# Kernel optimization log

Hardware: AMD Instinct MI355X
Metric: run time of the kernel (lower is better)

Reference implementation:

```python
import jax, jax.numpy as jnp
import numpy as np

B, A, C, M = 8, 32768, 80, 32
VAR0, VAR1 = 0.1, 0.2          # cfg['variance']
TOPK = 50                      # pre_anchor_topk
T1 = 0.5                       # bbox_threshold
SL1_W, SL1_B = 0.75, 0.11      # smooth_l1_loss_param
ALPHA, GAMMA = 0.5, 2.0
EPS = 1e-12


def point_form(b):
    # center form (cx,cy,w,h) -> corner form (x0,y0,x1,y1)
    return jnp.concatenate([b[..., :2] - b[..., 2:] / 2,
                            b[..., :2] + b[..., 2:] / 2], axis=-1)


def decode(loc, priors):
    xy = priors[..., :2] + loc[..., :2] * VAR0 * priors[..., 2:]
    wh = priors[..., 2:] * jnp.exp(loc[..., 2:] * VAR1)
    return jnp.concatenate([xy, wh], axis=-1)  # center form


def encode(matched, priors):
    # matched: corner form, priors: center form
    g_xy = ((matched[..., :2] + matched[..., 2:]) / 2 - priors[..., :2]) / (VAR0 * priors[..., 2:])
    g_wh = jnp.log((matched[..., 2:] - matched[..., :2]) / priors[..., 2:]) / VAR1
    return jnp.concatenate([g_xy, g_wh], axis=-1)


def jaccard(a, b):
    # a: [M,4] corner, b: [A,4] corner -> IoU [M,A]
    lt = jnp.maximum(a[:, None, :2], b[None, :, :2])
    rb = jnp.minimum(a[:, None, 2:], b[None, :, 2:])
    wh = jnp.clip(rb - lt, 0.0, None)
    inter = wh[..., 0] * wh[..., 1]
    area_a = (a[:, 2] - a[:, 0]) * (a[:, 3] - a[:, 1])
    area_b = (b[:, 2] - b[:, 0]) * (b[:, 3] - b[:, 1])
    return inter / (area_a[:, None] + area_b[None, :] - inter)


def clip_st(x, lo):
    # Clip custom Function: straight-through gradient
    return x + jax.lax.stop_gradient(jnp.maximum(x, lo) - x)


def bce_log(x):
    # torch BCE clamps log at -100
    return jnp.maximum(jnp.log(jnp.clip(x, 1e-38, None)), -100.0)


def _per_image(box_reg, cls_p, tgt, lab, anchors, num_classes):
    # ---- image_box_prob (no-grad branch in original) ----
    decoded = point_form(decode(box_reg, anchors))          # [A,4]
    obi = jaccard(tgt, decoded)                             # [M,A]
    t2 = jnp.maximum(obi.max(axis=1, keepdims=True), T1 + EPS)
    obp = jnp.clip((obi - T1) / (t2 - T1), 0.0, 1.0)        # [M,A]
    # sparse per-class max over objects == segment_max on labels
    seg = jax.ops.segment_max(obp, lab, num_segments=num_classes)  # [C,A]
    image_box_prob = jax.lax.stop_gradient(jnp.maximum(seg, 0.0).T)  # [A,C]

    # ---- positive bag loss ----
    mq = jaccard(tgt, point_form(anchors))                  # [M,A]
    _, matched = jax.lax.top_k(mq, TOPK)                    # [M,K]
    cls_sel = cls_p[:, lab].T                               # [M,A] prob of own class
    matched_cls = jnp.take_along_axis(cls_sel, matched, axis=1)  # [M,K]
    pri = anchors[matched]                                  # [M,K,4]
    tgt_enc = encode(tgt[:, None, :], pri)                  # [M,K,4]
    val = tgt_enc - box_reg[matched]
    av = jnp.abs(val)
    reg_loss = SL1_W * jnp.where(av < SL1_B, 0.5 / SL1_B * val * val, av - 0.5 * SL1_B).sum(-1)
    logits = matched_cls * jnp.exp(-reg_loss)               # [M,K]
    w = 1.0 / clip_st(1.0 - logits, EPS)
    w = w / w.sum(axis=1, keepdims=True)
    bag = (w * logits).sum(axis=1)                          # [M]
    pos = -bce_log(bag)                                     # BCE(bag, 1)
    return image_box_prob, pos


def setup_inputs() -> dict:
    key = jax.random.key(0)
    k1, k2, k3, k4, k5, k6, k7 = jax.random.split(key, 7)
    box_regression = jax.random.normal(k1, (B, A, 4), jnp.float32) * 0.5
    cls_logits = jax.random.normal(k2, (B, A, C), jnp.float32) - 2.0
    a_xy = jax.random.uniform(k3, (A, 2))
    a_wh = 0.02 + 0.2 * jax.random.uniform(k4, (A, 2))
    anchors = jnp.concatenate([a_xy, a_wh], axis=-1).astype(jnp.float32)
    t_min = 0.5 * jax.random.uniform(k5, (B, M, 2))
    t_wh = 0.05 + 0.4 * jax.random.uniform(k6, (B, M, 2))
    target_boxes = jnp.concatenate([t_min, t_min + t_wh], axis=-1).astype(jnp.float32)
    labels = jax.random.randint(k7, (B, M), 0, C, dtype=jnp.int32)
    return {"box_regression": box_regression, "cls_logits": cls_logits,
            "anchors": anchors, "target_boxes": target_boxes, "labels": labels}


def reference(box_regression, cls_logits, anchors, target_boxes, labels):
    num_classes = cls_logits.shape[-1]
    cls_prob = jax.nn.sigmoid(cls_logits)                   # [B,A,C]
    box_prob, pos = jax.vmap(
        lambda br, cp, tb, lb: _per_image(br, cp, tb, lb, anchors, num_classes)
    )(box_regression, cls_prob, target_boxes, labels)       # [B,A,C], [B,M]
    positive_numels = target_boxes.shape[0] * target_boxes.shape[1]
    positive_loss = pos.sum() / max(1, positive_numels)
    p = cls_prob * (1.0 - box_prob)
    # focal_loss(p, gamma) = sum(p**gamma * BCE(p, 0)) = sum(p**gamma * -log(1-p))
    negative_loss = jnp.sum(p ** GAMMA * (-bce_log(1.0 - p))) / max(1, positive_numels * TOPK)
    return (positive_loss * ALPHA, negative_loss * (1.0 - ALPHA))
```

## Files before the change

kernel.cpp:

```cpp
#include <hip/hip_runtime.h>

#define NB 8
#define NA 32768
#define NC 80
#define NM 32
#define NK 50
#define CAP 4096
#define TB 32
#define T2_BLOCKS (TB * NB)
#define POS_BLOCKS (NB * NM)
#define F0BLKS 512
#define CORRB (NA / 256)
constexpr float VAR0 = 0.1f, VAR1 = 0.2f;
constexpr float T1f  = 0.5f;
constexpr float SL1B = 0.11f;
constexpr float SL1W = 0.75f;
constexpr float FEPS = 1e-12f;

__device__ __forceinline__ float iou_corner(float tx0, float ty0, float tx1, float ty1, float ta,
                                            float bx0, float by0, float bx1, float by1, float ba) {
  float lx = fmaxf(tx0, bx0), ly = fmaxf(ty0, by0);
  float rx = fminf(tx1, bx1), ry = fminf(ty1, by1);
  float wx = fmaxf(rx - lx, 0.f), wy = fmaxf(ry - ly, 0.f);
  float inter = wx * wy;
  return inter / (ta + ba - inter);
}

__device__ __noinline__ float anchor_iou(float4 p, float tx0, float ty0, float tx1, float ty1, float ta) {
  float hx = 0.5f * p.z, hy = 0.5f * p.w;
  float x0 = p.x - hx, y0 = p.y - hy, x1 = p.x + hx, y1 = p.y + hy;
  float ba = (x1 - x0) * (y1 - y0);
  return iou_corner(tx0, ty0, tx1, ty1, ta, x0, y0, x1, y1, ba);
}

__device__ __forceinline__ float focal_term(float s, float bp) {
  float pr = s * (1.f - bp);
  float om = fmaxf(1.f - pr, 1e-38f);
  return pr * pr * fminf(-__logf(om), 100.f);
}

__global__ void __launch_bounds__(1024) mega_kernel(const float4* __restrict__ br,
                                                    const float* __restrict__ cls,
                                                    const float4* __restrict__ anc,
                                                    const float4* __restrict__ tgt,
                                                    const int* __restrict__ labels,
                                                    unsigned* __restrict__ partmax,
                                                    unsigned* __restrict__ pairmask,
                                                    float* __restrict__ posp,
                                                    float* __restrict__ f0part) {
  __shared__ int hist[512];
  __shared__ unsigned long long cand[CAP];
  __shared__ int sel[NK];
  __shared__ int s_cnt, s_B1, s_filled;
  __shared__ unsigned char s_flag[1024];
  __shared__ unsigned s_max[NM];
  __shared__ float4 s_t[NM];
  __shared__ float s_ta[NM];
  __shared__ float swave[16];

  int bx = blockIdx.x;
  int tid = threadIdx.x;

  if (bx < T2_BLOCKS) {
    int b = bx >> 5;
    int chunk = bx & 31;
    if (tid < NM) {
      float4 t = tgt[b * NM + tid];
      s_t[tid] = t;
      s_ta[tid] = (t.z - t.x) * (t.w - t.y);
      s_max[tid] = 0u;
    }
    __syncthreads();

    int a = chunk * 1024 + tid;
    float4 p = anc[a];
    float4 l = br[(size_t)b * NA + a];
    float cx = p.x + l.x * VAR0 * p.z;
    float cy = p.y + l.y * VAR0 * p.w;
    float w = p.z * __expf(l.z * VAR1);
    float h = p.w * __expf(l.w * VAR1);
    float dx0 = cx - 0.5f * w, dy0 = cy - 0.5f * h;
    float dx1 = cx + 0.5f * w, dy1 = cy + 0.5f * h;
    float da = (dx1 - dx0) * (dy1 - dy0);

    unsigned mymask = 0u;
#pragma unroll
    for (int mm = 0; mm < NM; ++mm) {
      int m = (tid + mm) & (NM - 1);
      float4 t = s_t[m];
      float iou = iou_corner(t.x, t.y, t.z, t.w, s_ta[m], dx0, dy0, dx1, dy1, da);
      if (iou > T1f) mymask |= 1u << m;
      atomicMax(&s_max[m], __float_as_uint(iou));
    }
    pairmask[(size_t)b * NA + a] = mymask;
    __syncthreads();
    if (tid < NM)
      partmax[((size_t)b * NM + tid) * TB + chunk] = s_max[tid];

  } else if (bx < T2_BLOCKS + POS_BLOCKS) {
    int bm = bx - T2_BLOCKS;
    int b = bm >> 5;
    float4 t = tgt[bm];
    float ta = (t.z - t.x) * (t.w - t.y);

    if (tid < 512) hist[tid] = 0;
    if (tid == 0) s_cnt = 0;
    __syncthreads();

    for (int a = tid; a < NA; a += 1024) {
      float iou = anchor_iou(anc[a], t.x, t.y, t.z, t.w, ta);
      if (iou > 0.f) {
        int bin = (int)(__float_as_uint(iou) >> 21);
        atomicAdd(&hist[bin], 1);
      }
    }
    __syncthreads();

    if (tid == 0) {
      int cum = 0, b1 = 0;
      for (int bin = 511; bin >= 0; --bin) {
        cum += hist[bin];
        if (cum >= NK) { b1 = bin; break; }
      }
      s_B1 = b1;
      s_filled = cum;
    }
    __syncthreads();
    int B1 = s_B1;
    bool zero_path = (s_filled < NK);

    for (int a = tid; a < NA; a += 1024) {
      float iou = anchor_iou(anc[a], t.x, t.y, t.z, t.w, ta);
      if (iou > 0.f) {
        unsigned vb = __float_as_uint(iou);
        if ((int)(vb >> 21) >= B1) {
          int slot = atomicAdd(&s_cnt, 1);
          if (slot < CAP)
            cand[slot] = ((unsigned long long)vb << 32) | (unsigned)(~a);
        }
      }
    }
    __syncthreads();
    int n = min(s_cnt, CAP);

    for (int c = tid; c < n; c += 1024) {
      unsigned long long key = cand[c];
      int rank = 0;
      for (int j = 0; j < n; ++j) rank += (cand[j] > key);
      if (rank < NK) sel[rank] = (int)(~(unsigned)(key & 0xFFFFFFFFull));
    }
    __syncthreads();

    if (zero_path) {
      if (tid == 0) s_filled = n;
      __syncthreads();
      for (int base = 0; base < NA; base += 1024) {
        int a = base + tid;
        float iou = anchor_iou(anc[a], t.x, t.y, t.z, t.w, ta);
        s_flag[tid] = (iou == 0.f);
        __syncthreads();
        if (tid == 0) {
          for (int i = 0; i < 1024 && s_filled < NK; ++i)
            if (s_flag[i]) { sel[s_filled++] = base + i; }
        }
        __syncthreads();
        if (s_filled >= NK) break;
      }
    }

    if (tid < 64) {
      int lane = tid;
      float lg = 0.f, wr = 0.f;
      if (lane < NK) {
        int a = sel[lane];
        int lb = labels[bm];
        float4 p = anc[a];
        float4 l = br[(size_t)b * NA + a];
        float logit = cls[((size_t)b * NA + a) * NC + lb];
        float mc = 1.f / (1.f + __expf(-logit));
        float gx = ((t.x + t.z) * 0.5f - p.x) / (VAR0 * p.z);
        float gy = ((t.y + t.w) * 0.5f - p.y) / (VAR0 * p.w);
        float gw = __logf((t.z - t.x) / p.z) / VAR1;
        float gh = __logf((t.w - t.y) / p.w) / VAR1;
        float v0 = gx - l.x, v1 = gy - l.y, v2 = gw - l.z, v3 = gh - l.w;
        float rl = 0.f;
        {
          float av;
          av = fabsf(v0); rl += (av < SL1B) ? (0.5f / SL1B) * v0 * v0 : (av - 0.5f * SL1B);
          av = fabsf(v1); rl += (av < SL1B) ? (0.5f / SL1B) * v1 * v1 : (av - 0.5f * SL1B);
          av = fabsf(v2); rl += (av < SL1B) ? (0.5f / SL1B) * v2 * v2 : (av - 0.5f * SL1B);
          av = fabsf(v3); rl += (av < SL1B) ? (0.5f / SL1B) * v3 * v3 : (av - 0.5f * SL1B);
        }
        rl *= SL1W;
        lg = mc * __expf(-rl);
        wr = 1.f / fmaxf(1.f - lg, FEPS);
      }
      float swl = wr * lg, swr = wr;
      for (int off = 32; off; off >>= 1) { swl += __shfl_down(swl, off); swr += __shfl_down(swr, off); }
      if (lane == 0) {
        float bag = swl / swr;
        posp[bm] = -fmaxf(logf(fmaxf(bag, 1e-38f)), -100.f);
      }
    }

  } else {
    int fb = bx - T2_BLOCKS - POS_BLOCKS;
    constexpr int NTOT4 = NB * NA * NC / 4;
    const float4* cls4 = (const float4*)cls;
    int stride = F0BLKS * 1024;
    float accum = 0.f;
    for (int i = fb * 1024 + tid; i < NTOT4; i += stride) {
      float4 v = cls4[i];
      float s0 = 1.f / (1.f + __expf(-v.x));
      float s1 = 1.f / (1.f + __expf(-v.y));
      float s2 = 1.f / (1.f + __expf(-v.z));
      float s3 = 1.f / (1.f + __expf(-v.w));
      accum += focal_term(s0, 0.f) + focal_term(s1, 0.f) +
               focal_term(s2, 0.f) + focal_term(s3, 0.f);
    }
    for (int off = 32; off; off >>= 1) accum += __shfl_down(accum, off);
    if ((tid & 63) == 0) swave[tid >> 6] = accum;
    __syncthreads();
    if (tid == 0) {
      float s = 0.f;
#pragma unroll
      for (int i = 0; i < 16; ++i) s += swave[i];
      f0part[fb] = s;
    }
  }
}

__global__ void __launch_bounds__(256) corr_kernel(const float4* __restrict__ br,
                                                   const float* __restrict__ cls,
                                                   const float4* __restrict__ anc,
                                                   const float4* __restrict__ tgt,
                                                   const int* __restrict__ labels,
                                                   const unsigned* __restrict__ partmax,
                                                   const unsigned* __restrict__ pairmask,
                                                   float* __restrict__ corrp) {
  __shared__ float4 s_t[NM];
  __shared__ float s_ta[NM], s_inv[NM];
  __shared__ unsigned s_cmask[NC];
  __shared__ unsigned s_maxm[NM];
  __shared__ unsigned s_slotmask[NM];
  __shared__ int s_slotclass[NM];
  __shared__ int s_nslots;
  int b = blockIdx.y;
  int tid = threadIdx.x;
  if (tid < NC) s_cmask[tid] = 0u;
  if (tid < NM) s_maxm[tid] = 0u;
  if (tid == 0) s_nslots = 0;
  __syncthreads();
  if (tid < NM) {
    float4 t = tgt[b * NM + tid];
    s_t[tid] = t;
    s_ta[tid] = (t.z - t.x) * (t.w - t.y);
    atomicOr(&s_cmask[labels[b * NM + tid]], 1u << tid);
  }
  {
    int m = tid >> 3, j = tid & 7;
    const unsigned* pm = &partmax[((size_t)b * NM + m) * TB];
    unsigned mx = 0u;
    for (int k = j; k < TB; k += 8) mx = max(mx, pm[k]);
    atomicMax(&s_maxm[m], mx);
  }
  __syncthreads();
  if (tid < NM) {
    float mxf = __uint_as_float(s_maxm[tid]);
    s_inv[tid] = 1.0f / (fmaxf(mxf, T1f) - T1f);
  }
  __syncthreads();
  if (tid < NC && s_cmask[tid] != 0u) {
    int slot = atomicAdd(&s_nslots, 1);
    s_slotmask[slot] = s_cmask[tid];
    s_slotclass[slot] = tid;
  }
  __syncthreads();
  int nslots = s_nslots;

  int a = blockIdx.x * 256 + tid;
  unsigned mk32 = pairmask[(size_t)b * NA + a];
  float accum = 0.f;
  if (mk32) {
    float4 p = anc[a];
    float4 l = br[(size_t)b * NA + a];
    float cx = p.x + l.x * VAR0 * p.z;
    float cy = p.y + l.y * VAR0 * p.w;
    float w = p.z * __expf(l.z * VAR1);
    float h = p.w * __expf(l.w * VAR1);
    float dx0 = cx - 0.5f * w, dy0 = cy - 0.5f * h;
    float dx1 = cx + 0.5f * w, dy1 = cy + 0.5f * h;
    float da = (dx1 - dx0) * (dy1 - dy0);
    for (int j = 0; j < nslots; ++j) {
      unsigned sm = mk32 & s_slotmask[j];
      if (!sm) continue;
      float bp = 0.f;
      while (sm) {
        int m = __ffs(sm) - 1;
        sm &= sm - 1;
        float4 t = s_t[m];
        float iou = iou_corner(t.x, t.y, t.z, t.w, s_ta[m], dx0, dy0, dx1, dy1, da);
        float o = (iou - T1f) * s_inv[m];
        bp = fmaxf(bp, fminf(fmaxf(o, 0.f), 1.f));
      }
      if (bp > 0.f) {
        float logit = cls[((size_t)b * NA + a) * NC + s_slotclass[j]];
        float s = 1.f / (1.f + __expf(-logit));
        accum += focal_term(s, bp) - focal_term(s, 0.f);
      }
    }
  }
  for (int off = 32; off; off >>= 1) accum += __shfl_down(accum, off);
  __shared__ float swv[4];
  if ((tid & 63) == 0) swv[tid >> 6] = accum;
  __syncthreads();
  if (tid == 0)
    corrp[(size_t)b * CORRB + blockIdx.x] = swv[0] + swv[1] + swv[2] + swv[3];
}

__global__ void __launch_bounds__(256) fin_kernel(const float* __restrict__ posp,
                                                  const float* __restrict__ f0part,
                                                  const float* __restrict__ corrp,
                                                  float* __restrict__ out) {
  int tid = threadIdx.x;
  double sp = 0.0, sn = 0.0;
  for (int i = tid; i < POS_BLOCKS; i += 256) sp += (double)posp[i];
  for (int i = tid; i < F0BLKS; i += 256) sn += (double)f0part[i];
  for (int i = tid; i < NB * CORRB; i += 256) sn += (double)corrp[i];
  for (int off = 32; off; off >>= 1) { sp += __shfl_down(sp, off); sn += __shfl_down(sn, off); }
  __shared__ double swp[4], swn[4];
  if ((tid & 63) == 0) { swp[tid >> 6] = sp; swn[tid >> 6] = sn; }
  __syncthreads();
  if (tid == 0) {
    double pos = swp[0] + swp[1] + swp[2] + swp[3];
    double neg = swn[0] + swn[1] + swn[2] + swn[3];
    out[0] = (float)(pos / 256.0 * 0.5);
    out[1] = (float)(neg / 12800.0 * 0.5);
  }
}

extern "C" void kernel_launch(void* const* d_in, const int* in_sizes, int n_in,
                              void* d_out, int out_size, void* d_ws, size_t ws_size,
                              hipStream_t stream) {
  const float4* br  = (const float4*)d_in[0];
  const float*  cls = (const float*)d_in[1];
  const float4* anc = (const float4*)d_in[2];
  const float4* tgt = (const float4*)d_in[3];
  const int*    lab = (const int*)d_in[4];
  float* out = (float*)d_out;
  float*    posp     = (float*)d_ws;
  float*    f0part   = (float*)((char*)d_ws + 4096);
  float*    corrp    = (float*)((char*)d_ws + 8192);
  unsigned* partmax  = (unsigned*)((char*)d_ws + 16384);
  unsigned* pairmask = (unsigned*)((char*)d_ws + 65536);

  mega_kernel<<<dim3(T2_BLOCKS + POS_BLOCKS + F0BLKS), 1024, 0, stream>>>(
      br, cls, anc, tgt, lab, partmax, pairmask, posp, f0part);
  corr_kernel<<<dim3(CORRB, NB), 256, 0, stream>>>(br, cls, anc, tgt, lab, partmax, pairmask, corrp);
  fin_kernel<<<1, 256, 0, stream>>>(posp, f0part, corrp, out);
}
```

Baseline: 60.13 us.

## Cache per-anchor IoUs in registers and schedule long positive blocks first

The positive-bag blocks now compute each anchor IoU once into a 32-entry register array and reuse it for the histogram, candidate collection and zero-fill passes, where before they recomputed it through a noinline call in each pass. The positive blocks are also moved to the front of the grid so these long-running blocks start first and overlap with the short IoU-max and focal blocks. A min-blocks hint is added to launch_bounds. The register array raises register pressure in a 1024-thread kernel that every branch shares, which may lower occupancy or cause spills.

```diff
diff --git a/kernel.cpp b/kernel.cpp
--- a/kernel.cpp
+++ b/kernel.cpp
@@ -7,8 +7,8 @@
 #define NK 50
 #define CAP 4096
 #define TB 32
+#define POS_BLOCKS (NB * NM)
 #define T2_BLOCKS (TB * NB)
-#define POS_BLOCKS (NB * NM)
 #define F0BLKS 512
 #define CORRB (NA / 256)
 constexpr float VAR0 = 0.1f, VAR1 = 0.2f;
@@ -26,28 +26,21 @@
   return inter / (ta + ba - inter);
 }
 
-__device__ __noinline__ float anchor_iou(float4 p, float tx0, float ty0, float tx1, float ty1, float ta) {
-  float hx = 0.5f * p.z, hy = 0.5f * p.w;
-  float x0 = p.x - hx, y0 = p.y - hy, x1 = p.x + hx, y1 = p.y + hy;
-  float ba = (x1 - x0) * (y1 - y0);
-  return iou_corner(tx0, ty0, tx1, ty1, ta, x0, y0, x1, y1, ba);
-}
-
 __device__ __forceinline__ float focal_term(float s, float bp) {
   float pr = s * (1.f - bp);
   float om = fmaxf(1.f - pr, 1e-38f);
   return pr * pr * fminf(-__logf(om), 100.f);
 }
 
-__global__ void __launch_bounds__(1024) mega_kernel(const float4* __restrict__ br,
-                                                    const float* __restrict__ cls,
-                                                    const float4* __restrict__ anc,
-                                                    const float4* __restrict__ tgt,
-                                                    const int* __restrict__ labels,
-                                                    unsigned* __restrict__ partmax,
-                                                    unsigned* __restrict__ pairmask,
-                                                    float* __restrict__ posp,
-                                                    float* __restrict__ f0part) {
+__global__ void __launch_bounds__(1024, 8) mega_kernel(const float4* __restrict__ br,
+                                                       const float* __restrict__ cls,
+                                                       const float4* __restrict__ anc,
+                                                       const float4* __restrict__ tgt,
+                                                       const int* __restrict__ labels,
+                                                       unsigned* __restrict__ partmax,
+                                                       unsigned* __restrict__ pairmask,
+                                                       float* __restrict__ posp,
+                                                       float* __restrict__ f0part) {
   __shared__ int hist[512];
   __shared__ unsigned long long cand[CAP];
   __shared__ int sel[NK];
@@ -61,44 +54,8 @@
   int bx = blockIdx.x;
   int tid = threadIdx.x;
 
-  if (bx < T2_BLOCKS) {
-    int b = bx >> 5;
-    int chunk = bx & 31;
-    if (tid < NM) {
-      float4 t = tgt[b * NM + tid];
-      s_t[tid] = t;
-      s_ta[tid] = (t.z - t.x) * (t.w - t.y);
-      s_max[tid] = 0u;
-    }
-    __syncthreads();
-
-    int a = chunk * 1024 + tid;
-    float4 p = anc[a];
-    float4 l = br[(size_t)b * NA + a];
-    float cx = p.x + l.x * VAR0 * p.z;
-    float cy = p.y + l.y * VAR0 * p.w;
-    float w = p.z * __expf(l.z * VAR1);
-    float h = p.w * __expf(l.w * VAR1);
-    float dx0 = cx - 0.5f * w, dy0 = cy - 0.5f * h;
-    float dx1 = cx + 0.5f * w, dy1 = cy + 0.5f * h;
-    float da = (dx1 - dx0) * (dy1 - dy0);
-
-    unsigned mymask = 0u;
-#pragma unroll
-    for (int mm = 0; mm < NM; ++mm) {
-      int m = (tid + mm) & (NM - 1);
-      float4 t = s_t[m];
-      float iou = iou_corner(t.x, t.y, t.z, t.w, s_ta[m], dx0, dy0, dx1, dy1, da);
-      if (iou > T1f) mymask |= 1u << m;
-      atomicMax(&s_max[m], __float_as_uint(iou));
-    }
-    pairmask[(size_t)b * NA + a] = mymask;
-    __syncthreads();
-    if (tid < NM)
-      partmax[((size_t)b * NM + tid) * TB + chunk] = s_max[tid];
-
-  } else if (bx < T2_BLOCKS + POS_BLOCKS) {
-    int bm = bx - T2_BLOCKS;
+  if (bx < POS_BLOCKS) {
+    int bm = bx;
     int b = bm >> 5;
     float4 t = tgt[bm];
     float ta = (t.z - t.x) * (t.w - t.y);
@@ -107,12 +64,16 @@
     if (tid == 0) s_cnt = 0;
     __syncthreads();
 
-    for (int a = tid; a < NA; a += 1024) {
-      float iou = anchor_iou(anc[a], t.x, t.y, t.z, t.w, ta);
-      if (iou > 0.f) {
-        int bin = (int)(__float_as_uint(iou) >> 21);
-        atomicAdd(&hist[bin], 1);
-      }
+    float riou[32];
+#pragma unroll
+    for (int k = 0; k < 32; ++k) {
+      float4 p = anc[tid + k * 1024];
+      float hx = 0.5f * p.z, hy = 0.5f * p.w;
+      float x0 = p.x - hx, y0 = p.y - hy, x1 = p.x + hx, y1 = p.y + hy;
+      float ba = (x1 - x0) * (y1 - y0);
+      float v = iou_corner(t.x, t.y, t.z, t.w, ta, x0, y0, x1, y1, ba);
+      riou[k] = v;
+      if (v > 0.f) atomicAdd(&hist[(int)(__float_as_uint(v) >> 21)], 1);
     }
     __syncthreads();
 
@@ -129,14 +90,15 @@
     int B1 = s_B1;
     bool zero_path = (s_filled < NK);
 
-    for (int a = tid; a < NA; a += 1024) {
-      float iou = anchor_iou(anc[a], t.x, t.y, t.z, t.w, ta);
-      if (iou > 0.f) {
-        unsigned vb = __float_as_uint(iou);
+#pragma unroll
+    for (int k = 0; k < 32; ++k) {
+      float v = riou[k];
+      if (v > 0.f) {
+        unsigned vb = __float_as_uint(v);
         if ((int)(vb >> 21) >= B1) {
           int slot = atomicAdd(&s_cnt, 1);
           if (slot < CAP)
-            cand[slot] = ((unsigned long long)vb << 32) | (unsigned)(~a);
+            cand[slot] = ((unsigned long long)vb << 32) | (unsigned)(~(tid + k * 1024));
         }
       }
     }
@@ -154,17 +116,18 @@
     if (zero_path) {
       if (tid == 0) s_filled = n;
       __syncthreads();
-      for (int base = 0; base < NA; base += 1024) {
-        int a = base + tid;
-        float iou = anchor_iou(anc[a], t.x, t.y, t.z, t.w, ta);
-        s_flag[tid] = (iou == 0.f);
-        __syncthreads();
-        if (tid == 0) {
-          for (int i = 0; i < 1024 && s_filled < NK; ++i)
-            if (s_flag[i]) { sel[s_filled++] = base + i; }
+#pragma unroll
+      for (int k = 0; k < 32; ++k) {
+        if (s_filled < NK) {
+          s_flag[tid] = (riou[k] == 0.f);
+          __syncthreads();
+          if (tid == 0) {
+            int base = k * 1024;
+            for (int i = 0; i < 1024 && s_filled < NK; ++i)
+              if (s_flag[i]) sel[s_filled++] = base + i;
+          }
+          __syncthreads();
         }
-        __syncthreads();
-        if (s_filled >= NK) break;
       }
     }
 
@@ -203,8 +166,45 @@
       }
     }
 
+  } else if (bx < POS_BLOCKS + T2_BLOCKS) {
+    int t2i = bx - POS_BLOCKS;
+    int b = t2i >> 5;
+    int chunk = t2i & 31;
+    if (tid < NM) {
+      float4 t = tgt[b * NM + tid];
+      s_t[tid] = t;
+      s_ta[tid] = (t.z - t.x) * (t.w - t.y);
+      s_max[tid] = 0u;
+    }
+    __syncthreads();
+
+    int a = chunk * 1024 + tid;
+    float4 p = anc[a];
+    float4 l = br[(size_t)b * NA + a];
+    float cx = p.x + l.x * VAR0 * p.z;
+    float cy = p.y + l.y * VAR0 * p.w;
+    float w = p.z * __expf(l.z * VAR1);
+    float h = p.w * __expf(l.w * VAR1);
+    float dx0 = cx - 0.5f * w, dy0 = cy - 0.5f * h;
+    float dx1 = cx + 0.5f * w, dy1 = cy + 0.5f * h;
+    float da = (dx1 - dx0) * (dy1 - dy0);
+
+    unsigned mymask = 0u;
+#pragma unroll
+    for (int mm = 0; mm < NM; ++mm) {
+      int m = (tid + mm) & (NM - 1);
+      float4 t = s_t[m];
+      float iou = iou_corner(t.x, t.y, t.z, t.w, s_ta[m], dx0, dy0, dx1, dy1, da);
+      if (iou > T1f) mymask |= 1u << m;
+      atomicMax(&s_max[m], __float_as_uint(iou));
+    }
+    pairmask[(size_t)b * NA + a] = mymask;
+    __syncthreads();
+    if (tid < NM)
+      partmax[((size_t)b * NM + tid) * TB + chunk] = s_max[tid];
+
   } else {
-    int fb = bx - T2_BLOCKS - POS_BLOCKS;
+    int fb = bx - POS_BLOCKS - T2_BLOCKS;
     constexpr int NTOT4 = NB * NA * NC / 4;
     const float4* cls4 = (const float4*)cls;
     int stride = F0BLKS * 1024;
@@ -354,7 +354,7 @@
   unsigned* partmax  = (unsigned*)((char*)d_ws + 16384);
   unsigned* pairmask = (unsigned*)((char*)d_ws + 65536);
 
-  mega_kernel<<<dim3(T2_BLOCKS + POS_BLOCKS + F0BLKS), 1024, 0, stream>>>(
+  mega_kernel<<<dim3(POS_BLOCKS + T2_BLOCKS + F0BLKS), 1024, 0, stream>>>(
       br, cls, anc, tgt, lab, partmax, pairmask, posp, f0part);
   corr_kernel<<<dim3(CORRB, NB), 256, 0, stream>>>(br, cls, anc, tgt, lab, partmax, pairmask, corrp);
   fin_kernel<<<1, 256, 0, stream>>>(posp, f0part, corrp, out);
```

Result: slower. 62.39 us (+3.8%).

## Distribute focal-sum streaming across all blocks before role-specific work

Applied to the files above, without the earlier changes.

The kernel no longer dedicates separate blocks to the dense focal sum. Every one of the 512 blocks now first streams a fixed slice of the class logits, with ten independent vector loads per thread, and reduces it. Each block then runs either the positive-bag or the IoU/mask work. This balances the heavy memory-bound sweep with the lighter per-anchor tasks and increases memory-level parallelism, at the cost of more registers and longer critical paths per block.

```diff
diff --git a/kernel.cpp b/kernel.cpp
--- a/kernel.cpp
+++ b/kernel.cpp
@@ -7,9 +7,7 @@
 #define NK 50
 #define CAP 4096
 #define TB 32
-#define T2_BLOCKS (TB * NB)
-#define POS_BLOCKS (NB * NM)
-#define F0BLKS 512
+#define NBLK 512
 #define CORRB (NA / 256)
 constexpr float VAR0 = 0.1f, VAR1 = 0.2f;
 constexpr float T1f  = 0.5f;
@@ -39,15 +37,23 @@
   return pr * pr * fminf(-__logf(om), 100.f);
 }
 
-__global__ void __launch_bounds__(1024) mega_kernel(const float4* __restrict__ br,
-                                                    const float* __restrict__ cls,
-                                                    const float4* __restrict__ anc,
-                                                    const float4* __restrict__ tgt,
-                                                    const int* __restrict__ labels,
-                                                    unsigned* __restrict__ partmax,
-                                                    unsigned* __restrict__ pairmask,
-                                                    float* __restrict__ posp,
-                                                    float* __restrict__ f0part) {
+__device__ __forceinline__ float focal4(float4 v) {
+  float s0 = 1.f / (1.f + __expf(-v.x));
+  float s1 = 1.f / (1.f + __expf(-v.y));
+  float s2 = 1.f / (1.f + __expf(-v.z));
+  float s3 = 1.f / (1.f + __expf(-v.w));
+  return focal_term(s0, 0.f) + focal_term(s1, 0.f) + focal_term(s2, 0.f) + focal_term(s3, 0.f);
+}
+
+__global__ void __launch_bounds__(1024, 8) mega_kernel(const float4* __restrict__ br,
+                                                       const float* __restrict__ cls,
+                                                       const float4* __restrict__ anc,
+                                                       const float4* __restrict__ tgt,
+                                                       const int* __restrict__ labels,
+                                                       unsigned* __restrict__ partmax,
+                                                       unsigned* __restrict__ pairmask,
+                                                       float* __restrict__ posp,
+                                                       float* __restrict__ f0part) {
   __shared__ int hist[512];
   __shared__ unsigned long long cand[CAP];
   __shared__ int sel[NK];
@@ -61,44 +67,36 @@
   int bx = blockIdx.x;
   int tid = threadIdx.x;
 
-  if (bx < T2_BLOCKS) {
-    int b = bx >> 5;
-    int chunk = bx & 31;
-    if (tid < NM) {
-      float4 t = tgt[b * NM + tid];
-      s_t[tid] = t;
-      s_ta[tid] = (t.z - t.x) * (t.w - t.y);
-      s_max[tid] = 0u;
-    }
-    __syncthreads();
-
-    int a = chunk * 1024 + tid;
-    float4 p = anc[a];
-    float4 l = br[(size_t)b * NA + a];
-    float cx = p.x + l.x * VAR0 * p.z;
-    float cy = p.y + l.y * VAR0 * p.w;
-    float w = p.z * __expf(l.z * VAR1);
-    float h = p.w * __expf(l.w * VAR1);
-    float dx0 = cx - 0.5f * w, dy0 = cy - 0.5f * h;
-    float dx1 = cx + 0.5f * w, dy1 = cy + 0.5f * h;
-    float da = (dx1 - dx0) * (dy1 - dy0);
-
-    unsigned mymask = 0u;
+  {
+    const float4* cls4 = (const float4*)cls;
+    constexpr int STRIDE = NBLK * 1024;
+    int base = bx * 1024 + tid;
+    float4 v0 = cls4[base + 0 * STRIDE];
+    float4 v1 = cls4[base + 1 * STRIDE];
+    float4 v2 = cls4[base + 2 * STRIDE];
+    float4 v3 = cls4[base + 3 * STRIDE];
+    float4 v4 = cls4[base + 4 * STRIDE];
+    float accum = focal4(v0) + focal4(v1) + focal4(v2) + focal4(v3) + focal4(v4);
+    float4 w0 = cls4[base + 5 * STRIDE];
+    float4 w1 = cls4[base + 6 * STRIDE];
+    float4 w2 = cls4[base + 7 * STRIDE];
+    float4 w3 = cls4[base + 8 * STRIDE];
+    float4 w4 = cls4[base + 9 * STRIDE];
+    accum += focal4(w0) + focal4(w1) + focal4(w2) + focal4(w3) + focal4(w4);
+    for (int off = 32; off; off >>= 1) accum += __shfl_down(accum, off);
+    if ((tid & 63) == 0) swave[tid >> 6] = accum;
+    __syncthreads();
+    if (tid == 0) {
+      float s = 0.f;
 #pragma unroll
-    for (int mm = 0; mm < NM; ++mm) {
-      int m = (tid + mm) & (NM - 1);
-      float4 t = s_t[m];
-      float iou = iou_corner(t.x, t.y, t.z, t.w, s_ta[m], dx0, dy0, dx1, dy1, da);
-      if (iou > T1f) mymask |= 1u << m;
-      atomicMax(&s_max[m], __float_as_uint(iou));
-    }
-    pairmask[(size_t)b * NA + a] = mymask;
-    __syncthreads();
-    if (tid < NM)
-      partmax[((size_t)b * NM + tid) * TB + chunk] = s_max[tid];
-
-  } else if (bx < T2_BLOCKS + POS_BLOCKS) {
-    int bm = bx - T2_BLOCKS;
+      for (int i = 0; i < 16; ++i) s += swave[i];
+      f0part[bx] = s;
+    }
+    __syncthreads();
+  }
+
+  if (bx < NB * NM) {
+    int bm = bx;
     int b = bm >> 5;
     float4 t = tgt[bm];
     float ta = (t.z - t.x) * (t.w - t.y);
@@ -204,29 +202,41 @@
     }
 
   } else {
-    int fb = bx - T2_BLOCKS - POS_BLOCKS;
-    constexpr int NTOT4 = NB * NA * NC / 4;
-    const float4* cls4 = (const float4*)cls;
-    int stride = F0BLKS * 1024;
-    float accum = 0.f;
-    for (int i = fb * 1024 + tid; i < NTOT4; i += stride) {
-      float4 v = cls4[i];
-      float s0 = 1.f / (1.f + __expf(-v.x));
-      float s1 = 1.f / (1.f + __expf(-v.y));
-      float s2 = 1.f / (1.f + __expf(-v.z));
-      float s3 = 1.f / (1.f + __expf(-v.w));
-      accum += focal_term(s0, 0.f) + focal_term(s1, 0.f) +
-               focal_term(s2, 0.f) + focal_term(s3, 0.f);
-    }
-    for (int off = 32; off; off >>= 1) accum += __shfl_down(accum, off);
-    if ((tid & 63) == 0) swave[tid >> 6] = accum;
-    __syncthreads();
-    if (tid == 0) {
-      float s = 0.f;
+    int t2i = bx - NB * NM;
+    int b = t2i >> 5;
+    int chunk = t2i & 31;
+    if (tid < NM) {
+      float4 t = tgt[b * NM + tid];
+      s_t[tid] = t;
+      s_ta[tid] = (t.z - t.x) * (t.w - t.y);
+      s_max[tid] = 0u;
+    }
+    __syncthreads();
+
+    int a = chunk * 1024 + tid;
+    float4 p = anc[a];
+    float4 l = br[(size_t)b * NA + a];
+    float cx = p.x + l.x * VAR0 * p.z;
+    float cy = p.y + l.y * VAR0 * p.w;
+    float w = p.z * __expf(l.z * VAR1);
+    float h = p.w * __expf(l.w * VAR1);
+    float dx0 = cx - 0.5f * w, dy0 = cy - 0.5f * h;
+    float dx1 = cx + 0.5f * w, dy1 = cy + 0.5f * h;
+    float da = (dx1 - dx0) * (dy1 - dy0);
+
+    unsigned mymask = 0u;
 #pragma unroll
-      for (int i = 0; i < 16; ++i) s += swave[i];
-      f0part[fb] = s;
-    }
+    for (int mm = 0; mm < NM; ++mm) {
+      int m = (tid + mm) & (NM - 1);
+      float4 t = s_t[m];
+      float iou = iou_corner(t.x, t.y, t.z, t.w, s_ta[m], dx0, dy0, dx1, dy1, da);
+      if (iou > T1f) mymask |= 1u << m;
+      atomicMax(&s_max[m], __float_as_uint(iou));
+    }
+    pairmask[(size_t)b * NA + a] = mymask;
+    __syncthreads();
+    if (tid < NM)
+      partmax[((size_t)b * NM + tid) * TB + chunk] = s_max[tid];
   }
 }
 
@@ -324,8 +334,8 @@
                                                   float* __restrict__ out) {
   int tid = threadIdx.x;
   double sp = 0.0, sn = 0.0;
-  for (int i = tid; i < POS_BLOCKS; i += 256) sp += (double)posp[i];
-  for (int i = tid; i < F0BLKS; i += 256) sn += (double)f0part[i];
+  for (int i = tid; i < NB * NM; i += 256) sp += (double)posp[i];
+  for (int i = tid; i < NBLK; i += 256) sn += (double)f0part[i];
   for (int i = tid; i < NB * CORRB; i += 256) sn += (double)corrp[i];
   for (int off = 32; off; off >>= 1) { sp += __shfl_down(sp, off); sn += __shfl_down(sn, off); }
   __shared__ double swp[4], swn[4];
@@ -354,7 +364,7 @@
   unsigned* partmax  = (unsigned*)((char*)d_ws + 16384);
   unsigned* pairmask = (unsigned*)((char*)d_ws + 65536);
 
-  mega_kernel<<<dim3(T2_BLOCKS + POS_BLOCKS + F0BLKS), 1024, 0, stream>>>(
+  mega_kernel<<<dim3(NBLK), 1024, 0, stream>>>(
       br, cls, anc, tgt, lab, partmax, pairmask, posp, f0part);
   corr_kernel<<<dim3(CORRB, NB), 256, 0, stream>>>(br, cls, anc, tgt, lab, partmax, pairmask, corrp);
   fin_kernel<<<1, 256, 0, stream>>>(posp, f0part, corrp, out);
```

New measurement: 58.57 us. 2.6% less time.
